# Performance work log

Measured on AMD Instinct MI355X. Metric: run time of the kernel, lower is better.

Reference implementation:

```python
import jax, jax.numpy as jnp
import numpy as np

D_DEC = 256  # decoder_size; W columns are [decoder | encoder] per the torch concat order


def setup_inputs() -> dict:
    key = jax.random.key(0)
    k1, k2, k3, k4 = jax.random.split(key, 4)
    B, S, E, D, A = 32, 4096, 256, 256, 256
    decoder_hidden = jax.random.normal(k1, (1, B, D), dtype=jnp.float32)
    encoder_outputs = jax.random.normal(k2, (S, B, E), dtype=jnp.float32)
    W = jax.random.normal(k3, (A, D + E), dtype=jnp.float32) / np.sqrt(D + E)
    b = jax.random.normal(k4, (A,), dtype=jnp.float32) * 0.02
    return {"decoder_hidden": decoder_hidden, "encoder_outputs": encoder_outputs, "W": W, "b": b}


def reference(decoder_hidden, encoder_outputs, W, b):
    # decoder_hidden: [1,B,D] -> [B,D]; encoder_outputs: [S,B,E] -> [B,S,E]
    dh = decoder_hidden[0]
    eo = jnp.transpose(encoder_outputs, (1, 0, 2))
    # Split the concat-linear: cat([dec, enc]) @ W.T == dec @ Wd.T + enc @ We.T
    Wd, We = W[:, :D_DEC], W[:, D_DEC:]
    # scores: tanh(linear) summed over attn dim -> [B,S]
    proj = dh @ Wd.T + b  # [B,A]
    attn = jnp.tanh(proj[:, None, :] + jnp.einsum('bse,ae->bsa', eo, We))
    scores = jnp.sum(attn, axis=2)  # [B,S]
    attn_softmax = jax.nn.softmax(scores, axis=1)  # [B,S]
    attended = jnp.einsum('bs,bse->be', attn_softmax, eo)  # [B,E]
    encoder_norms = jnp.linalg.norm(eo, axis=2)  # [B,S]
    attn_map = attn_softmax * encoder_norms
    return attended, attn_map
```

## Files before the change

### kernel.cpp

```cpp
#include <hip/hip_runtime.h>
#include <math.h>

#define B_  32
#define S_  4096
#define E_  256
#define A_  256
#define DE_ 512
#define SCH 128

typedef __attribute__((ext_vector_type(8))) short short8;
typedef __attribute__((ext_vector_type(4))) float f32x4;

__device__ inline unsigned short f2bf(float x) {
    unsigned int u = __float_as_uint(x);
    u += 0x7FFFu + ((u >> 16) & 1u);
    return (unsigned short)(u >> 16);
}
__device__ inline float bf2f(unsigned short h) {
    return __uint_as_float(((unsigned int)h) << 16);
}
__device__ inline float tanh_fast(float x) {
    x = fminf(fmaxf(x, -15.f), 15.f);
    float t = __expf(2.f * x);
    return (t - 1.f) / (t + 1.f);
}

__global__ __launch_bounds__(256) void wprep_kernel(
    const float* __restrict__ W, unsigned short* __restrict__ wepk)
{
    const int idx = blockIdx.x * 256 + threadIdx.x;
    const int c     = idx >> 11;
    const int r     = idx & 2047;
    const int plane = r >> 10;
    const int kg    = (r >> 8) & 3;
    const int a     = r & 255;
    const float* src = W + (size_t)a * DE_ + E_ + c * 32 + kg * 8;
    unsigned int pk[4];
    #pragma unroll
    for (int j = 0; j < 4; ++j) {
        float x0 = src[2 * j], x1 = src[2 * j + 1];
        unsigned short h0 = f2bf(x0), h1 = f2bf(x1);
        unsigned short v0 = plane ? f2bf(x0 - bf2f(h0)) : h0;
        unsigned short v1 = plane ? f2bf(x1 - bf2f(h1)) : h1;
        pk[j] = (unsigned int)v0 | ((unsigned int)v1 << 16);
    }
    *(uint4*)&wepk[(size_t)idx * 8] = make_uint4(pk[0], pk[1], pk[2], pk[3]);
}

__global__ __launch_bounds__(256) void proj_kernel(
    const float* __restrict__ dh, const float* __restrict__ W,
    const float* __restrict__ bias, float* __restrict__ proj)
{
    __shared__ float dh_lds[E_];
    const int b = blockIdx.x;
    const int a = threadIdx.x;
    dh_lds[a] = dh[b * E_ + a];
    __syncthreads();
    float acc = bias[a];
    const float* wrow = W + (size_t)a * DE_;
    #pragma unroll
    for (int d = 0; d < E_; d += 4) {
        float4 w = *(const float4*)(wrow + d);
        acc += dh_lds[d] * w.x + dh_lds[d+1] * w.y
             + dh_lds[d+2] * w.z + dh_lds[d+3] * w.w;
    }
    proj[b * A_ + a] = acc;
}

__global__ __launch_bounds__(256, 3) void scores_kernel(
    const float* __restrict__ eo,
    const unsigned short* __restrict__ wepk,
    const float* __restrict__ proj,
    float* __restrict__ scores, float* __restrict__ nsq)
{
    __shared__ __align__(16) unsigned short we_hl[2 * 4 * 256 * 8];
    __shared__ __align__(16) unsigned short eo_hl[2 * 4 * 64 * 8];
    __shared__ float proj_lds[A_];
    __shared__ float npart[512];

    const int tid = threadIdx.x;
    const int b   = blockIdx.x & (B_ - 1);
    const int s0  = (blockIdx.x / B_) * 64;
    const int w   = tid >> 6;
    const int l   = tid & 63;
    const int lq  = l >> 4;
    const int lr  = l & 15;

    proj_lds[tid] = proj[b * A_ + tid];

    f32x4 acc[4][4];
    #pragma unroll
    for (int i = 0; i < 4; ++i)
        #pragma unroll
        for (int j = 0; j < 4; ++j)
            acc[i][j] = (f32x4){0.f, 0.f, 0.f, 0.f};

    const int erow0 = tid >> 3;
    const int ekq   = tid & 7;
    const int ekg   = ekq >> 1, ehalf = ekq & 1;
    float nacc[2] = {0.f, 0.f};

    for (int kc = 0, c = 0; kc < E_; kc += 32, ++c) {
        __syncthreads();
        #pragma unroll
        for (int it = 0; it < 2; ++it) {
            const int row = it * 32 + erow0;
            float4 v = *(const float4*)(eo + (size_t)(s0 + row) * (B_ * E_)
                                           + b * E_ + kc + ekq * 4);
            nacc[it] += v.x*v.x + v.y*v.y + v.z*v.z + v.w*v.w;
            unsigned short h0 = f2bf(v.x), h1 = f2bf(v.y);
            unsigned short h2 = f2bf(v.z), h3 = f2bf(v.w);
            unsigned int hp0 = (unsigned int)h0 | ((unsigned int)h1 << 16);
            unsigned int hp1 = (unsigned int)h2 | ((unsigned int)h3 << 16);
            unsigned int lp0 = (unsigned int)f2bf(v.x - bf2f(h0))
                             | ((unsigned int)f2bf(v.y - bf2f(h1)) << 16);
            unsigned int lp1 = (unsigned int)f2bf(v.z - bf2f(h2))
                             | ((unsigned int)f2bf(v.w - bf2f(h3)) << 16);
            const int u = ekg * 64 + row;
            *(uint2*)&eo_hl[(size_t)u * 8 + ehalf * 4]         = make_uint2(hp0, hp1);
            *(uint2*)&eo_hl[(size_t)(256 + u) * 8 + ehalf * 4] = make_uint2(lp0, lp1);
        }
        const unsigned short* gsrc = wepk + (size_t)c * 2048 * 8;
        #pragma unroll
        for (int it = 0; it < 8; ++it) {
            const int u = it * 256 + tid;
            __builtin_amdgcn_global_load_lds(
                (const __attribute__((address_space(1))) void*)(gsrc + (size_t)u * 8),
                (__attribute__((address_space(3))) void*)&we_hl[(size_t)u * 8],
                16, 0, 0);
        }
        __syncthreads();
        short8 bh[4], bl[4];
        #pragma unroll
        for (int nt = 0; nt < 4; ++nt) {
            int bunit = lq * 256 + w * 64 + nt * 16 + lr;
            bh[nt] = *(const short8*)&we_hl[(size_t)bunit * 8];
            bl[nt] = *(const short8*)&we_hl[(size_t)(1024 + bunit) * 8];
        }
        #pragma unroll
        for (int mt = 0; mt < 4; ++mt) {
            int aunit = lq * 64 + mt * 16 + lr;
            short8 ah = *(const short8*)&eo_hl[(size_t)aunit * 8];
            short8 al = *(const short8*)&eo_hl[(size_t)(256 + aunit) * 8];
            #pragma unroll
            for (int nt = 0; nt < 4; ++nt) {
                acc[mt][nt] = __builtin_amdgcn_mfma_f32_16x16x32_bf16(ah, bh[nt], acc[mt][nt], 0, 0, 0);
                acc[mt][nt] = __builtin_amdgcn_mfma_f32_16x16x32_bf16(ah, bl[nt], acc[mt][nt], 0, 0, 0);
                acc[mt][nt] = __builtin_amdgcn_mfma_f32_16x16x32_bf16(al, bh[nt], acc[mt][nt], 0, 0, 0);
            }
        }
    }
    __syncthreads();

    float* red4 = (float*)we_hl;
    float pr[4];
    #pragma unroll
    for (int nt = 0; nt < 4; ++nt) pr[nt] = proj_lds[w * 64 + nt * 16 + lr];
    #pragma unroll
    for (int mt = 0; mt < 4; ++mt) {
        #pragma unroll
        for (int r = 0; r < 4; ++r) {
            float s = 0.f;
            #pragma unroll
            for (int nt = 0; nt < 4; ++nt)
                s += tanh_fast(pr[nt] + acc[mt][nt][r]);
            red4[(w * 16 + lr) * 65 + (mt * 16 + lq * 4 + r)] = s;
        }
    }
    npart[tid]       = nacc[0];
    npart[256 + tid] = nacc[1];
    __syncthreads();
    if (tid < 64) {
        float s = 0.f;
        #pragma unroll 8
        for (int c2 = 0; c2 < 64; ++c2) s += red4[c2 * 65 + tid];
        scores[b * S_ + s0 + tid] = s;
        const int base = (tid >> 5) * 256 + (tid & 31) * 8;
        float nq = 0.f;
        #pragma unroll
        for (int q = 0; q < 8; ++q) nq += npart[base + q];
        nsq[b * S_ + s0 + tid] = nq;
    }
}

__global__ __launch_bounds__(256) void softmax_kernel(
    float* __restrict__ nsq_p, float* __restrict__ out)
{
    __shared__ float red[256];
    const int b = blockIdx.x;
    const int tid = threadIdx.x;
    float* scores = out + B_ * E_;

    float v[16];
    float m = -1e30f;
    #pragma unroll
    for (int i = 0; i < 16; ++i) {
        v[i] = scores[b * S_ + i * 256 + tid];
        m = fmaxf(m, v[i]);
    }
    red[tid] = m;
    __syncthreads();
    for (int off = 128; off > 0; off >>= 1) {
        if (tid < off) red[tid] = fmaxf(red[tid], red[tid + off]);
        __syncthreads();
    }
    m = red[0];
    __syncthreads();
    float sum = 0.f;
    #pragma unroll
    for (int i = 0; i < 16; ++i) { v[i] = expf(v[i] - m); sum += v[i]; }
    red[tid] = sum;
    __syncthreads();
    for (int off = 128; off > 0; off >>= 1) {
        if (tid < off) red[tid] += red[tid + off];
        __syncthreads();
    }
    const float inv = 1.f / red[0];
    #pragma unroll
    for (int i = 0; i < 16; ++i) {
        int s = i * 256 + tid;
        float pp = v[i] * inv;
        float nq = nsq_p[b * S_ + s];
        nsq_p[b * S_ + s] = pp;
        scores[b * S_ + s] = pp * sqrtf(nq);
    }
    out[b * E_ + tid] = 0.f;
}

__global__ __launch_bounds__(256) void attend_kernel(
    const float* __restrict__ eo, const float* __restrict__ p,
    float* __restrict__ out)
{
    __shared__ float4 red[4][64];
    const int tid = threadIdx.x;
    const int b   = blockIdx.x & (B_ - 1);
    const int ch  = blockIdx.x / B_;
    const int le  = tid & 63;
    const int sg  = tid >> 6;
    const int s0  = ch * SCH + sg * (SCH / 4);
    float4 acc = make_float4(0.f, 0.f, 0.f, 0.f);
    #pragma unroll 4
    for (int s = 0; s < SCH / 4; ++s) {
        float pv = p[b * S_ + s0 + s];
        float4 v = *(const float4*)(eo + (size_t)(s0 + s) * (B_ * E_)
                                       + b * E_ + le * 4);
        acc.x = fmaf(pv, v.x, acc.x);
        acc.y = fmaf(pv, v.y, acc.y);
        acc.z = fmaf(pv, v.z, acc.z);
        acc.w = fmaf(pv, v.w, acc.w);
    }
    red[sg][le] = acc;
    __syncthreads();
    if (tid < 64) {
        float4 a0 = red[0][tid], a1 = red[1][tid];
        float4 a2 = red[2][tid], a3 = red[3][tid];
        float* dst = out + b * E_ + tid * 4;
        atomicAdd(dst + 0, a0.x + a1.x + a2.x + a3.x);
        atomicAdd(dst + 1, a0.y + a1.y + a2.y + a3.y);
        atomicAdd(dst + 2, a0.z + a1.z + a2.z + a3.z);
        atomicAdd(dst + 3, a0.w + a1.w + a2.w + a3.w);
    }
}

extern "C" void kernel_launch(void* const* d_in, const int* in_sizes, int n_in,
                              void* d_out, int out_size, void* d_ws, size_t ws_size,
                              hipStream_t stream)
{
    const float* dh   = (const float*)d_in[0];
    const float* eo   = (const float*)d_in[1];
    const float* W    = (const float*)d_in[2];
    const float* bias = (const float*)d_in[3];
    float* out = (float*)d_out;
    float* ws  = (float*)d_ws;

    float* projb = ws;
    float* nsqp  = ws + 8192;
    unsigned short* wepk = (unsigned short*)(ws + 8192 + S_ * B_);
    float* scores = out + B_ * E_;

    wprep_kernel  <<<16384 / 256,     256, 0, stream>>>(W, wepk);
    proj_kernel   <<<B_,              256, 0, stream>>>(dh, W, bias, projb);
    scores_kernel <<<B_ * (S_ / 64),  256, 0, stream>>>(eo, wepk, projb, scores, nsqp);
    softmax_kernel<<<B_,              256, 0, stream>>>(nsqp, out);
    attend_kernel <<<B_ * (S_ / SCH), 256, 0, stream>>>(eo, nsqp, out);
}
```

Before: 272.0 us.

## Cut LDS use, swizzle eo tile, truncate hi split, raise occupancy

The bf16 hi/lo split now truncates for the high part instead of rounding, which removes ALU work in the staging loop. The eo LDS tile is XOR-swizzled to reduce bank conflicts on the MFMA operand reads. proj is loaded straight into registers, and npart now reuses the we_hl buffer instead of its own shared arrays, which frees LDS so launch bounds can go from 3 to 4 blocks per CU. The final score reduction is split across all four waves, and tanh uses a hardware reciprocal. Truncation shifts the hi/lo split (the lo term still carries the residual), and the higher occupancy target may cause register spills.

Result: no change. 268.5 us (-1.3%).

```diff
diff --git a/kernel.cpp b/kernel.cpp
--- a/kernel.cpp
+++ b/kernel.cpp
@@ -22,7 +22,7 @@
 __device__ inline float tanh_fast(float x) {
     x = fminf(fmaxf(x, -15.f), 15.f);
     float t = __expf(2.f * x);
-    return (t - 1.f) / (t + 1.f);
+    return (t - 1.f) * __builtin_amdgcn_rcpf(t + 1.f);
 }
 
 __global__ __launch_bounds__(256) void wprep_kernel(
@@ -39,10 +39,15 @@
     #pragma unroll
     for (int j = 0; j < 4; ++j) {
         float x0 = src[2 * j], x1 = src[2 * j + 1];
-        unsigned short h0 = f2bf(x0), h1 = f2bf(x1);
-        unsigned short v0 = plane ? f2bf(x0 - bf2f(h0)) : h0;
-        unsigned short v1 = plane ? f2bf(x1 - bf2f(h1)) : h1;
-        pk[j] = (unsigned int)v0 | ((unsigned int)v1 << 16);
+        unsigned int u0 = __float_as_uint(x0) & 0xFFFF0000u;
+        unsigned int u1 = __float_as_uint(x1) & 0xFFFF0000u;
+        if (plane) {
+            unsigned short l0 = f2bf(x0 - __uint_as_float(u0));
+            unsigned short l1 = f2bf(x1 - __uint_as_float(u1));
+            pk[j] = (unsigned int)l0 | ((unsigned int)l1 << 16);
+        } else {
+            pk[j] = (u0 >> 16) | u1;
+        }
     }
     *(uint4*)&wepk[(size_t)idx * 8] = make_uint4(pk[0], pk[1], pk[2], pk[3]);
 }
@@ -67,7 +72,7 @@
     proj[b * A_ + a] = acc;
 }
 
-__global__ __launch_bounds__(256, 3) void scores_kernel(
+__global__ __launch_bounds__(256, 4) void scores_kernel(
     const float* __restrict__ eo,
     const unsigned short* __restrict__ wepk,
     const float* __restrict__ proj,
@@ -75,8 +80,6 @@
 {
     __shared__ __align__(16) unsigned short we_hl[2 * 4 * 256 * 8];
     __shared__ __align__(16) unsigned short eo_hl[2 * 4 * 64 * 8];
-    __shared__ float proj_lds[A_];
-    __shared__ float npart[512];
 
     const int tid = threadIdx.x;
     const int b   = blockIdx.x & (B_ - 1);
@@ -85,8 +88,11 @@
     const int l   = tid & 63;
     const int lq  = l >> 4;
     const int lr  = l & 15;
-
-    proj_lds[tid] = proj[b * A_ + tid];
+    const int lqx = (lq & 1) << 2;
+
+    float pr[4];
+    #pragma unroll
+    for (int nt = 0; nt < 4; ++nt) pr[nt] = proj[b * A_ + w * 64 + nt * 16 + lr];
 
     f32x4 acc[4][4];
     #pragma unroll
@@ -98,6 +104,7 @@
     const int erow0 = tid >> 3;
     const int ekq   = tid & 7;
     const int ekg   = ekq >> 1, ehalf = ekq & 1;
+    const int esw   = (ekg & 1) << 2;
     float nacc[2] = {0.f, 0.f};
 
     for (int kc = 0, c = 0; kc < E_; kc += 32, ++c) {
@@ -108,15 +115,17 @@
             float4 v = *(const float4*)(eo + (size_t)(s0 + row) * (B_ * E_)
                                            + b * E_ + kc + ekq * 4);
             nacc[it] += v.x*v.x + v.y*v.y + v.z*v.z + v.w*v.w;
-            unsigned short h0 = f2bf(v.x), h1 = f2bf(v.y);
-            unsigned short h2 = f2bf(v.z), h3 = f2bf(v.w);
-            unsigned int hp0 = (unsigned int)h0 | ((unsigned int)h1 << 16);
-            unsigned int hp1 = (unsigned int)h2 | ((unsigned int)h3 << 16);
-            unsigned int lp0 = (unsigned int)f2bf(v.x - bf2f(h0))
-                             | ((unsigned int)f2bf(v.y - bf2f(h1)) << 16);
-            unsigned int lp1 = (unsigned int)f2bf(v.z - bf2f(h2))
-                             | ((unsigned int)f2bf(v.w - bf2f(h3)) << 16);
-            const int u = ekg * 64 + row;
+            unsigned int ux = __float_as_uint(v.x) & 0xFFFF0000u;
+            unsigned int uy = __float_as_uint(v.y) & 0xFFFF0000u;
+            unsigned int uz = __float_as_uint(v.z) & 0xFFFF0000u;
+            unsigned int uw = __float_as_uint(v.w) & 0xFFFF0000u;
+            unsigned int hp0 = (ux >> 16) | uy;
+            unsigned int hp1 = (uz >> 16) | uw;
+            unsigned int lp0 = (unsigned int)f2bf(v.x - __uint_as_float(ux))
+                             | ((unsigned int)f2bf(v.y - __uint_as_float(uy)) << 16);
+            unsigned int lp1 = (unsigned int)f2bf(v.z - __uint_as_float(uz))
+                             | ((unsigned int)f2bf(v.w - __uint_as_float(uw)) << 16);
+            const int u = ekg * 64 + (row ^ esw);
             *(uint2*)&eo_hl[(size_t)u * 8 + ehalf * 4]         = make_uint2(hp0, hp1);
             *(uint2*)&eo_hl[(size_t)(256 + u) * 8 + ehalf * 4] = make_uint2(lp0, lp1);
         }
@@ -139,7 +148,7 @@
         }
         #pragma unroll
         for (int mt = 0; mt < 4; ++mt) {
-            int aunit = lq * 64 + mt * 16 + lr;
+            int aunit = lq * 64 + ((mt * 16 + lr) ^ lqx);
             short8 ah = *(const short8*)&eo_hl[(size_t)aunit * 8];
             short8 al = *(const short8*)&eo_hl[(size_t)(256 + aunit) * 8];
             #pragma unroll
@@ -152,10 +161,9 @@
     }
     __syncthreads();
 
-    float* red4 = (float*)we_hl;
-    float pr[4];
-    #pragma unroll
-    for (int nt = 0; nt < 4; ++nt) pr[nt] = proj_lds[w * 64 + nt * 16 + lr];
+    float* red4  = (float*)we_hl;
+    float* npart = red4 + 64 * 65;
+    float* qpart = npart + 512;
     #pragma unroll
     for (int mt = 0; mt < 4; ++mt) {
         #pragma unroll
@@ -170,15 +178,21 @@
     npart[tid]       = nacc[0];
     npart[256 + tid] = nacc[1];
     __syncthreads();
+    {
+        const int r = tid & 63, q = tid >> 6;
+        float s = 0.f;
+        #pragma unroll
+        for (int c2 = q * 16; c2 < q * 16 + 16; ++c2) s += red4[c2 * 65 + r];
+        qpart[q * 64 + r] = s;
+    }
+    __syncthreads();
     if (tid < 64) {
-        float s = 0.f;
-        #pragma unroll 8
-        for (int c2 = 0; c2 < 64; ++c2) s += red4[c2 * 65 + tid];
-        scores[b * S_ + s0 + tid] = s;
+        scores[b * S_ + s0 + tid] = qpart[tid] + qpart[64 + tid]
+                                  + qpart[128 + tid] + qpart[192 + tid];
         const int base = (tid >> 5) * 256 + (tid & 31) * 8;
         float nq = 0.f;
         #pragma unroll
-        for (int q = 0; q < 8; ++q) nq += npart[base + q];
+        for (int q2 = 0; q2 < 8; ++q2) nq += npart[base + q2];
         nsq[b * S_ + s0 + tid] = nq;
     }
 }
```
